# Kernel optimization log

Hardware: AMD Instinct MI355X
Metric: run time of the kernel (lower is better)

Reference implementation:

```python
import jax, jax.numpy as jnp
import numpy as np

B, T_DEC, T_ENC = 64, 400, 512
D = 256    # embed_size (GRU units, attention units, attention_layer_size)
PRE = 128  # prenet output dim (Tacotron prenet: 256 -> 128)
OUT = 400  # n_mels * r = 80 * 5


def _p(k, shape, s=0.05):
    return jax.random.normal(k, shape, dtype=jnp.float32) * s


def setup_inputs() -> dict:
    ks = jax.random.split(jax.random.key(0), 16)
    return {
        "dec_inputs": jax.random.normal(ks[0], (B, T_DEC, OUT), dtype=jnp.float32),
        "memory": jax.random.normal(ks[1], (B, T_ENC, D), dtype=jnp.float32),
        "W1": _p(ks[2], (OUT, D)), "b1": jnp.zeros((D,), jnp.float32),
        "W2": _p(ks[3], (D, PRE)), "b2": jnp.zeros((PRE,), jnp.float32),
        "k0": _p(ks[4], (PRE + D, 3 * D)), "r0": _p(ks[5], (D, 3 * D)),
        "bi0": jnp.zeros((3 * D,), jnp.float32), "br0": jnp.zeros((3 * D,), jnp.float32),
        "k1": _p(ks[6], (D, 3 * D)), "r1": _p(ks[7], (D, 3 * D)),
        "bi1": jnp.zeros((3 * D,), jnp.float32), "br1": jnp.zeros((3 * D,), jnp.float32),
        "Wq": _p(ks[8], (D, D)), "Wm": _p(ks[9], (D, D)), "v": _p(ks[10], (D,)),
        "Wa": _p(ks[11], (2 * D, D)),
        "Wo": _p(ks[12], (D, OUT)), "bo": jnp.zeros((OUT,), jnp.float32),
    }


def _gru(x, h, Wk, Wr, bi, br):
    # Keras GRUCell (reset_after=True)
    gx = x @ Wk + bi
    gh = h @ Wr + br
    xz, xr, xh = jnp.split(gx, 3, axis=-1)
    hz, hr, hh = jnp.split(gh, 3, axis=-1)
    z = jax.nn.sigmoid(xz + hz)
    r = jax.nn.sigmoid(xr + hr)
    hcand = jnp.tanh(xh + r * hh)
    return z * h + (1.0 - z) * hcand


def reference(dec_inputs, memory, W1, b1, W2, b2, k0, r0, bi0, br0,
              k1, r1, bi1, br1, Wq, Wm, v, Wa, Wo, bo):
    # Prenet (teacher forcing -> can apply to all steps up front). Dropout is
    # identity in eval mode.
    p = jax.nn.relu(jax.nn.relu(dec_inputs @ W1 + b1) @ W2 + b2)  # [B,Td,PRE]
    keys = memory @ Wm  # Bahdanau memory layer, precomputed  [B,Te,D]
    b = dec_inputs.shape[0]
    h0 = jnp.zeros((b, D), dec_inputs.dtype)
    h1 = jnp.zeros((b, D), dec_inputs.dtype)
    att0 = jnp.zeros((b, D), dec_inputs.dtype)

    def step(carry, x):
        h0, h1, att = carry
        cin = jnp.concatenate([x, att], axis=-1)           # [B, PRE+D]
        h0n = _gru(cin, h0, k0, r0, bi0, br0)
        h1n = _gru(h0n, h1, k1, r1, bi1, br1)              # cell output
        q = h1n @ Wq                                        # query layer
        score = jnp.einsum('btd,d->bt', jnp.tanh(keys + q[:, None, :]), v)
        alpha = jax.nn.softmax(score, axis=-1)              # [B,Te]
        ctx = jnp.einsum('bt,btd->bd', alpha, memory)       # context
        attn = jnp.concatenate([h1n, ctx], axis=-1) @ Wa    # attention layer
        y = attn @ Wo + bo                                  # output Dense
        return (h0n, h1n, attn), y

    _, ys = jax.lax.scan(step, (h0, h1, att0), jnp.swapaxes(p, 0, 1))
    return jnp.swapaxes(ys, 0, 1)  # [B, T_DEC, OUT]
```

## Files before the change

kernel.cpp:

```cpp
#include <hip/hip_runtime.h>
#include <hip/hip_fp16.h>

#define BB   64
#define TDEC 400
#define TENC 512
#define DD   256
#define PRE  128
#define NOUT 400
#define G3   768
#define C2E  2.8853900817779268f

typedef _Float16 h2_t __attribute__((ext_vector_type(2)));

__device__ __forceinline__ float fsig(float x) {
    return __builtin_amdgcn_rcpf(1.0f + __expf(-x));
}
__device__ __forceinline__ float ftanh(float x) {
    float t = __expf(2.0f * x);
    return 1.0f - 2.0f * __builtin_amdgcn_rcpf(t + 1.0f);
}
__device__ __forceinline__ float fexp2(float x) {
#if __has_builtin(__builtin_amdgcn_exp2f)
    return __builtin_amdgcn_exp2f(x);
#else
    return exp2f(x);
#endif
}
__device__ __forceinline__ float dot8(float4 w, float4 x, float acc) {
    union { float4 f; h2_t h[4]; } uw, ux;
    uw.f = w; ux.f = x;
#if __has_builtin(__builtin_amdgcn_fdot2)
    #pragma unroll
    for (int k = 0; k < 4; k++)
        acc = __builtin_amdgcn_fdot2(uw.h[k], ux.h[k], acc, false);
#else
    #pragma unroll
    for (int k = 0; k < 4; k++) {
        acc = fmaf((float)uw.h[k].x, (float)ux.h[k].x, acc);
        acc = fmaf((float)uw.h[k].y, (float)ux.h[k].y, acc);
    }
#endif
    return acc;
}

__global__ __launch_bounds__(256) void prenet_kernel(
    const float* __restrict__ x, const float* __restrict__ W1, const float* __restrict__ b1,
    const float* __restrict__ W2, const float* __restrict__ b2, __half* __restrict__ p_h)
{
    __shared__ __align__(16) float xs[8][NOUT];
    __shared__ __align__(16) float hs[8][DD];
    const int row0 = blockIdx.x * 8;
    const int tid = threadIdx.x;
    for (int idx = tid; idx < 8 * NOUT; idx += 256) {
        int m = idx / NOUT, i = idx - m * NOUT;
        xs[m][i] = x[(size_t)(row0 + m) * NOUT + i];
    }
    __syncthreads();
    {
        const int j = tid;
        float acc[8];
        float bj = b1[j];
        #pragma unroll
        for (int m = 0; m < 8; m++) acc[m] = bj;
        #pragma unroll 4
        for (int i = 0; i < NOUT; i++) {
            float w = W1[i * DD + j];
            #pragma unroll
            for (int m = 0; m < 8; m++) acc[m] = fmaf(xs[m][i], w, acc[m]);
        }
        #pragma unroll
        for (int m = 0; m < 8; m++) hs[m][j] = fmaxf(acc[m], 0.0f);
    }
    __syncthreads();
    if (tid < PRE) {
        const int j = tid;
        float acc[8];
        float bj = b2[j];
        #pragma unroll
        for (int m = 0; m < 8; m++) acc[m] = bj;
        #pragma unroll 4
        for (int i = 0; i < DD; i++) {
            float w = W2[i * PRE + j];
            #pragma unroll
            for (int m = 0; m < 8; m++) acc[m] = fmaf(hs[m][i], w, acc[m]);
        }
        #pragma unroll
        for (int m = 0; m < 8; m++)
            p_h[(size_t)(row0 + m) * PRE + j] = __float2half(fmaxf(acc[m], 0.0f));
    }
}

__global__ __launch_bounds__(768) void gx0_kernel(
    const __half* __restrict__ p_h, const float* __restrict__ k0,
    const float* __restrict__ bi0, __half* __restrict__ gxp)
{
    __shared__ __align__(16) float ps[8][PRE];
    const int row0 = blockIdx.x * 8;
    const int tid = threadIdx.x;
    for (int idx = tid; idx < 8 * PRE; idx += 768) {
        int m = idx >> 7, i = idx & 127;
        ps[m][i] = __half2float(p_h[(size_t)(row0 + m) * PRE + i]);
    }
    __syncthreads();
    const int j = tid;
    float acc[8];
    float bj = bi0[j];
    #pragma unroll
    for (int m = 0; m < 8; m++) acc[m] = bj;
    #pragma unroll 4
    for (int i = 0; i < PRE; i++) {
        float w = k0[(size_t)i * G3 + j];
        #pragma unroll
        for (int m = 0; m < 8; m++) acc[m] = fmaf(ps[m][i], w, acc[m]);
    }
    #pragma unroll
    for (int m = 0; m < 8; m++)
        gxp[(size_t)(row0 + m) * G3 + j] = __float2half(acc[m]);
}

__global__ __launch_bounds__(256) void keys_kernel(
    const float* __restrict__ mem, const float* __restrict__ Wm, __half* __restrict__ keys_p)
{
    __shared__ __align__(16) float xs[8][DD];
    const int row0 = blockIdx.x * 8;
    const int tid = threadIdx.x;
    for (int idx = tid; idx < 8 * DD; idx += 256) {
        int m = idx >> 8, i = idx & 255;
        xs[m][i] = mem[(size_t)(row0 + m) * DD + i];
    }
    __syncthreads();
    const int j = tid;
    const int i8 = j >> 3, k = j & 7;
    float acc[8] = {0.f,0.f,0.f,0.f,0.f,0.f,0.f,0.f};
    #pragma unroll 4
    for (int i = 0; i < DD; i++) {
        float w = Wm[i * DD + j];
        #pragma unroll
        for (int m = 0; m < 8; m++) acc[m] = fmaf(xs[m][i], w, acc[m]);
    }
    #pragma unroll
    for (int m = 0; m < 8; m++) {
        int r = row0 + m;
        int bb = r >> 9, e = r & 511;
        keys_p[(size_t)bb * (TENC * DD) + ((size_t)i8 * TENC + e) * 8 + k] =
            __float2half(C2E * acc[m]);
    }
}

__global__ __launch_bounds__(256) void pack_w_kernel(
    const float* __restrict__ src, __half* __restrict__ dst, int R, int C)
{
    int flat = blockIdx.x * 256 + threadIdx.x;
    if (flat < R * C) {
        int k = flat & 7;
        int t2 = flat >> 3;
        int j = t2 % C;
        int i8 = t2 / C;
        dst[flat] = __float2half(src[(size_t)(8 * i8 + k) * C + j]);
    }
}

__global__ __launch_bounds__(256) void pack_mem8_kernel(
    const float* __restrict__ mem, float4* __restrict__ dst)
{
    int flat = blockIdx.x * 256 + threadIdx.x;
    if (flat < BB * 64 * 256) {
        int d  = flat & 255;
        int e8 = (flat >> 8) & 63;
        int b  = flat >> 14;
        const float* base = mem + ((size_t)b * TENC + 8 * e8) * DD + d;
        union { float4 f; __half2 h[4]; } u;
        u.h[0] = __floats2half2_rn(base[0 * DD], base[1 * DD]);
        u.h[1] = __floats2half2_rn(base[2 * DD], base[3 * DD]);
        u.h[2] = __floats2half2_rn(base[4 * DD], base[5 * DD]);
        u.h[3] = __floats2half2_rn(base[6 * DD], base[7 * DD]);
        dst[flat] = u.f;
    }
}

__global__ __launch_bounds__(448) void out_kernel(
    const __half* __restrict__ ah, const float* __restrict__ Wo, const float* __restrict__ bo,
    float* __restrict__ y)
{
    __shared__ __align__(16) float xs[8][DD];
    const int row0 = blockIdx.x * 8;
    const int tid = threadIdx.x;
    for (int idx = tid; idx < 8 * DD; idx += 448) {
        int m = idx >> 8, i = idx & 255;
        xs[m][i] = __half2float(ah[(size_t)(row0 + m) * DD + i]);
    }
    __syncthreads();
    if (tid < NOUT) {
        const int j = tid;
        float acc[8];
        float bj = bo[j];
        #pragma unroll
        for (int m = 0; m < 8; m++) acc[m] = bj;
        #pragma unroll 4
        for (int i = 0; i < DD; i++) {
            float w = Wo[i * NOUT + j];
            #pragma unroll
            for (int m = 0; m < 8; m++) acc[m] = fmaf(xs[m][i], w, acc[m]);
        }
        #pragma unroll
        for (int m = 0; m < 8; m++) y[(size_t)(row0 + m) * NOUT + j] = acc[m];
    }
}

#define SCORE_BODY(UK) do {                                              \
    float4 q0 = qp4[2 * i8], q1 = qp4[2 * i8 + 1];                       \
    float4 v0 = vp4[2 * i8], v1 = vp4[2 * i8 + 1];                       \
    float a0 = (float)UK.h[0].x + q0.x;                                  \
    float a1 = (float)UK.h[0].y + q0.y;                                  \
    float a2 = (float)UK.h[1].x + q0.z;                                  \
    float a3 = (float)UK.h[1].y + q0.w;                                  \
    float a4 = (float)UK.h[2].x + q1.x;                                  \
    float a5 = (float)UK.h[2].y + q1.y;                                  \
    float a6 = (float)UK.h[3].x + q1.z;                                  \
    float a7 = (float)UK.h[3].y + q1.w;                                  \
    accA = fmaf(v0.x, __builtin_amdgcn_rcpf(fexp2(a0) + 1.0f), accA);    \
    accB = fmaf(v0.y, __builtin_amdgcn_rcpf(fexp2(a1) + 1.0f), accB);    \
    accA = fmaf(v0.z, __builtin_amdgcn_rcpf(fexp2(a2) + 1.0f), accA);    \
    accB = fmaf(v0.w, __builtin_amdgcn_rcpf(fexp2(a3) + 1.0f), accB);    \
    accA = fmaf(v1.x, __builtin_amdgcn_rcpf(fexp2(a4) + 1.0f), accA);    \
    accB = fmaf(v1.y, __builtin_amdgcn_rcpf(fexp2(a5) + 1.0f), accB);    \
    accA = fmaf(v1.z, __builtin_amdgcn_rcpf(fexp2(a6) + 1.0f), accA);    \
    accB = fmaf(v1.w, __builtin_amdgcn_rcpf(fexp2(a7) + 1.0f), accB);    \
} while (0)

__global__ __launch_bounds__(768, 1) void decoder_kernel(
    const __half* __restrict__ gxp,  const __half* __restrict__ keys_p,
    const float4* __restrict__ memq,
    const __half* __restrict__ k0p,  const __half* __restrict__ r0p,
    const __half* __restrict__ k1p,  const __half* __restrict__ r1p,
    const __half* __restrict__ Wqp,  const __half* __restrict__ Wap,
    const float* __restrict__ br0,
    const float* __restrict__ bi1, const float* __restrict__ br1,
    const float* __restrict__ v,   __half* __restrict__ ahist)
{
    __shared__ __align__(16) float4 kLds4[16 * TENC];
    __shared__ __align__(16) __half xa[DD];
    __shared__ __align__(16) __half h0s[DD], h1s[DD];
    __shared__ __align__(16) __half ctxh[DD];
    __shared__ __align__(16) float h0f[DD], h1f[DD];
    __shared__ __align__(16) float qf[DD], vf[DD];
    __shared__ __align__(16) float gx[G3], gh[G3];
    __shared__ __align__(16) float sc[TENC];
    __shared__ __align__(16) float hWa[DD];
    __shared__ __align__(16) float ctxp[3][DD];
    __shared__ __align__(16) float redd[16];

    const int tid = threadIdx.x;
    const int b = blockIdx.x;

    const float b0r_r = br0[tid];
    const float b1i_r = bi1[tid];
    const float b1r_r = br1[tid];
    if (tid < DD) {
        h0f[tid] = 0.0f; h1f[tid] = 0.0f;
        h0s[tid] = __float2half(0.0f); h1s[tid] = __float2half(0.0f);
        vf[tid] = v[tid];
        xa[tid] = __float2half(0.0f);
    }
    const __half*  keyb = keys_p + (size_t)b * TENC * DD;
    const float4*  kg4  = (const float4*)keyb;
    const float4*  mqb  = memq + (size_t)b * (TENC / 8) * DD;
    const __half*  gxb  = gxp + (size_t)b * TDEC * G3;

    {
        const float4* src = (const float4*)keyb;
        for (int idx = tid; idx < 16 * TENC; idx += 768)
            kLds4[idx] = src[16 * TENC + idx];
    }

    __half gpre = gxb[tid];
    __syncthreads();

    #pragma unroll 1
    for (int t = 0; t < TDEC; t++) {
        {
            const float4* wpA = (const float4*)k0p;
            const float4* wpB = (const float4*)r0p;
            const float4* xp  = (const float4*)xa;
            const float4* hp  = (const float4*)h0s;
            float acc  = __half2float(gpre);
            if (t + 1 < TDEC) gpre = gxb[(size_t)(t + 1) * G3 + tid];
            float acc2 = b0r_r;
            #pragma unroll 4
            for (int i8 = 0; i8 < 32; i8++) {
                float4 x = xp[i8], h = hp[i8];
                acc  = dot8(wpA[(16 + i8) * G3 + tid], x, acc);
                acc2 = dot8(wpB[i8 * G3 + tid], h, acc2);
            }
            gx[tid] = acc; gh[tid] = acc2;
        }
        __syncthreads();
        if (tid < DD) {
            float z = fsig(gx[tid] + gh[tid]);
            float r = fsig(gx[DD + tid] + gh[DD + tid]);
            float cand = ftanh(gx[2 * DD + tid] + r * gh[2 * DD + tid]);
            float hn = z * h0f[tid] + (1.0f - z) * cand;
            h0f[tid] = hn; h0s[tid] = __float2half(hn);
        }
        __syncthreads();

        {
            const float4* wpA = (const float4*)k1p;
            const float4* wpB = (const float4*)r1p;
            const float4* xp  = (const float4*)h0s;
            const float4* hp  = (const float4*)h1s;
            float acc  = b1i_r;
            float acc2 = b1r_r;
            #pragma unroll 4
            for (int i8 = 0; i8 < 32; i8++) {
                float4 x = xp[i8], h = hp[i8];
                acc  = dot8(wpA[i8 * G3 + tid], x, acc);
                acc2 = dot8(wpB[i8 * G3 + tid], h, acc2);
            }
            gx[tid] = acc; gh[tid] = acc2;
        }
        __syncthreads();
        if (tid < DD) {
            float z = fsig(gx[tid] + gh[tid]);
            float r = fsig(gx[DD + tid] + gh[DD + tid]);
            float cand = ftanh(gx[2 * DD + tid] + r * gh[2 * DD + tid]);
            float hn = z * h1f[tid] + (1.0f - z) * cand;
            h1f[tid] = hn; h1s[tid] = __float2half(hn);
        }
        __syncthreads();

        if (tid < 256) {
            const float4* wp = (const float4*)Wqp;
            const float4* hp = (const float4*)h1s;
            float a0 = 0.0f, a1 = 0.0f;
            #pragma unroll 4
            for (int i8 = 0; i8 < 32; i8 += 2) {
                a0 = dot8(wp[i8 * DD + tid], hp[i8], a0);
                a1 = dot8(wp[(i8 + 1) * DD + tid], hp[i8 + 1], a1);
            }
            qf[tid] = C2E * (a0 + a1);
        } else if (tid < 512) {
            const int d = tid - 256;
            const float4* wp = (const float4*)Wap;
            const float4* hp = (const float4*)h1s;
            float a0 = 0.0f, a1 = 0.0f;
            #pragma unroll 4
            for (int i8 = 0; i8 < 32; i8 += 2) {
                a0 = dot8(wp[i8 * DD + d], hp[i8], a0);
                a1 = dot8(wp[(i8 + 1) * DD + d], hp[i8 + 1], a1);
            }
            hWa[d] = a0 + a1;
        }
        __syncthreads();

        if (tid < TENC) {
            const float4* qp4 = (const float4*)qf;
            const float4* vp4 = (const float4*)vf;
            float accA = 0.0f, accB = 0.0f;
            #pragma unroll 8
            for (int i8 = 0; i8 < 16; i8++) {
                union { float4 f; h2_t h[4]; } uk;
                uk.f = kg4[i8 * TENC + tid];
                SCORE_BODY(uk);
            }
            #pragma unroll 4
            for (int i8 = 16; i8 < 32; i8++) {
                union { float4 f; h2_t h[4]; } uk;
                uk.f = kLds4[(i8 - 16) * TENC + tid];
                SCORE_BODY(uk);
            }
            float wv = __expf(-2.0f * (accA + accB));
            sc[tid] = wv;
            #pragma unroll
            for (int off = 32; off; off >>= 1) wv += __shfl_down(wv, off);
            if ((tid & 63) == 0) redd[tid >> 6] = wv;
        }
        __syncthreads();

        {
            const int d  = tid & 255;
            const int ch = tid >> 8;
            const int e8s = (ch == 0) ? 0 : (ch == 1) ? 22 : 43;
            const int e8e = (ch == 0) ? 22 : (ch == 1) ? 43 : 64;
            const float4* scp = (const float4*)sc;
            float acc = 0.0f;
            #pragma unroll 2
            for (int e8 = e8s; e8 < e8e; e8++) {
                union { float4 f; __half2 h[4]; } um;
                um.f = mqb[e8 * DD + d];
                float4 w0 = scp[2 * e8], w1 = scp[2 * e8 + 1];
                float2 f0 = __half22float2(um.h[0]), f1 = __half22float2(um.h[1]);
                float2 f2 = __half22float2(um.h[2]), f3 = __half22float2(um.h[3]);
                acc = fmaf(f0.x, w0.x, acc); acc = fmaf(f0.y, w0.y, acc);
                acc = fmaf(f1.x, w0.z, acc); acc = fmaf(f1.y, w0.w, acc);
                acc = fmaf(f2.x, w1.x, acc); acc = fmaf(f2.y, w1.y, acc);
                acc = fmaf(f3.x, w1.z, acc); acc = fmaf(f3.y, w1.w, acc);
            }
            ctxp[ch][d] = acc;
        }
        __syncthreads();

        if (tid < DD) {
            const float4* rp = (const float4*)redd;
            float4 ra = rp[0], rb = rp[1];
            float ssum = ((ra.x + ra.y) + (ra.z + ra.w)) + ((rb.x + rb.y) + (rb.z + rb.w));
            float c = (ctxp[0][tid] + ctxp[1][tid] + ctxp[2][tid]) * __builtin_amdgcn_rcpf(ssum);
            ctxh[tid] = __float2half(c);
        }
        __syncthreads();

        if (tid < DD) {
            const float4* wp = (const float4*)Wap;
            const float4* cp = (const float4*)ctxh;
            float a0 = hWa[tid], a1 = 0.0f;
            #pragma unroll 4
            for (int i8 = 0; i8 < 32; i8 += 2) {
                a0 = dot8(wp[(32 + i8) * DD + tid], cp[i8], a0);
                a1 = dot8(wp[(33 + i8) * DD + tid], cp[i8 + 1], a1);
            }
            __half ah = __float2half(a0 + a1);
            xa[tid] = ah;
            ahist[((size_t)b * TDEC + t) * DD + tid] = ah;
        }
        __syncthreads();
    }
}

extern "C" void kernel_launch(void* const* d_in, const int* in_sizes, int n_in,
                              void* d_out, int out_size, void* d_ws, size_t ws_size,
                              hipStream_t stream)
{
    const float* dec    = (const float*)d_in[0];
    const float* memory = (const float*)d_in[1];
    const float* W1  = (const float*)d_in[2];
    const float* b1  = (const float*)d_in[3];
    const float* W2  = (const float*)d_in[4];
    const float* b2  = (const float*)d_in[5];
    const float* k0  = (const float*)d_in[6];
    const float* r0  = (const float*)d_in[7];
    const float* bi0 = (const float*)d_in[8];
    const float* br0 = (const float*)d_in[9];
    const float* k1  = (const float*)d_in[10];
    const float* r1  = (const float*)d_in[11];
    const float* bi1 = (const float*)d_in[12];
    const float* br1 = (const float*)d_in[13];
    const float* Wq  = (const float*)d_in[14];
    const float* Wm  = (const float*)d_in[15];
    const float* v   = (const float*)d_in[16];
    const float* Wa  = (const float*)d_in[17];
    const float* Wo  = (const float*)d_in[18];
    const float* bo  = (const float*)d_in[19];
    float* out = (float*)d_out;
    (void)ws_size; (void)in_sizes; (void)n_in; (void)out_size;

    char* w = (char*)d_ws;
    size_t off = 0;
    __half*  p_h    = (__half*)(w + off);  off += (size_t)BB * TDEC * PRE * 2;
    __half*  keys_p = (__half*)(w + off);  off += (size_t)BB * TENC * DD * 2;
    float4*  memq   = (float4*)(w + off);  off += (size_t)BB * TENC * DD * 2;
    __half*  gxp    = (__half*)(w + off);  off += (size_t)BB * TDEC * G3 * 2;
    __half*  k0p    = (__half*)(w + off);  off += (size_t)384 * G3 * 2;
    __half*  r0p    = (__half*)(w + off);  off += (size_t)DD * G3 * 2;
    __half*  k1p    = (__half*)(w + off);  off += (size_t)DD * G3 * 2;
    __half*  r1p    = (__half*)(w + off);  off += (size_t)DD * G3 * 2;
    __half*  Wqp    = (__half*)(w + off);  off += (size_t)DD * DD * 2;
    __half*  Wap    = (__half*)(w + off);  off += (size_t)2 * DD * DD * 2;
    __half*  ahist  = (__half*)(w + off);  off += (size_t)BB * TDEC * DD * 2;

    prenet_kernel<<<BB * TDEC / 8, 256, 0, stream>>>(dec, W1, b1, W2, b2, p_h);
    gx0_kernel<<<BB * TDEC / 8, 768, 0, stream>>>(p_h, k0, bi0, gxp);
    keys_kernel<<<BB * TENC / 8, 256, 0, stream>>>(memory, Wm, keys_p);
    pack_mem8_kernel<<<(BB * 64 * 256) / 256, 256, 0, stream>>>(memory, memq);
    pack_w_kernel<<<(384 * G3 + 255) / 256, 256, 0, stream>>>(k0, k0p, 384, G3);
    pack_w_kernel<<<(DD * G3 + 255) / 256, 256, 0, stream>>>(r0, r0p, DD, G3);
    pack_w_kernel<<<(DD * G3 + 255) / 256, 256, 0, stream>>>(k1, k1p, DD, G3);
    pack_w_kernel<<<(DD * G3 + 255) / 256, 256, 0, stream>>>(r1, r1p, DD, G3);
    pack_w_kernel<<<(DD * DD + 255) / 256, 256, 0, stream>>>(Wq, Wqp, DD, DD);
    pack_w_kernel<<<(2 * DD * DD + 255) / 256, 256, 0, stream>>>(Wa, Wap, 2 * DD, DD);

    decoder_kernel<<<BB, 768, 0, stream>>>(gxp, keys_p, memq, k0p, r0p, k1p, r1p,
                                           Wqp, Wap, br0, bi1, br1, v, ahist);

    out_kernel<<<BB * TDEC / 8, 448, 0, stream>>>(ahist, Wo, bo, out);
}
```

Measured before the change: 14.28 ms.

## Split each batch decoder across two blocks exchanging partial context via global mailboxes

```diff
diff --git a/kernel.cpp b/kernel.cpp
--- a/kernel.cpp
+++ b/kernel.cpp
@@ -236,22 +236,29 @@
     const __half* __restrict__ Wqp,  const __half* __restrict__ Wap,
     const float* __restrict__ br0,
     const float* __restrict__ bi1, const float* __restrict__ br1,
-    const float* __restrict__ v,   __half* __restrict__ ahist)
-{
-    __shared__ __align__(16) float4 kLds4[16 * TENC];
+    const float* __restrict__ v,   __half* __restrict__ ahist,
+    float* __restrict__ mboxC, float* __restrict__ mboxS,
+    unsigned* __restrict__ flags)
+{
+    __shared__ __align__(16) float4 kAll[32 * 256];
     __shared__ __align__(16) __half xa[DD];
     __shared__ __align__(16) __half h0s[DD], h1s[DD];
     __shared__ __align__(16) __half ctxh[DD];
     __shared__ __align__(16) float h0f[DD], h1f[DD];
     __shared__ __align__(16) float qf[DD], vf[DD];
     __shared__ __align__(16) float gx[G3], gh[G3];
-    __shared__ __align__(16) float sc[TENC];
+    __shared__ __align__(16) float sc[256];
     __shared__ __align__(16) float hWa[DD];
     __shared__ __align__(16) float ctxp[3][DD];
-    __shared__ __align__(16) float redd[16];
+    __shared__ __align__(16) float redd[8];
 
     const int tid = threadIdx.x;
-    const int b = blockIdx.x;
+    const int idxb = blockIdx.x;
+    const int g    = idxb >> 4;
+    const int sub  = idxb & 15;
+    const int who  = sub >> 3;
+    const int b    = g * 8 + (sub & 7);
+    const int eBase = who * 256;
 
     const float b0r_r = br0[tid];
     const float b1i_r = bi1[tid];
@@ -267,10 +274,16 @@
     const float4*  mqb  = memq + (size_t)b * (TENC / 8) * DD;
     const __half*  gxb  = gxp + (size_t)b * TDEC * G3;
 
-    {
-        const float4* src = (const float4*)keyb;
-        for (int idx = tid; idx < 16 * TENC; idx += 768)
-            kLds4[idx] = src[16 * TENC + idx];
+    float* mcOwn  = mboxC + ((size_t)(b * 2 + who) * 2) * 256;
+    float* mcPeer = mboxC + ((size_t)(b * 2 + (who ^ 1)) * 2) * 256;
+    float* msOwn  = mboxS + (b * 2 + who) * 2;
+    float* msPeer = mboxS + (b * 2 + (who ^ 1)) * 2;
+    unsigned* flagOwn  = flags + (b * 2 + who);
+    unsigned* flagPeer = flags + (b * 2 + (who ^ 1));
+
+    for (int i2 = tid; i2 < 32 * 256; i2 += 768) {
+        int i8 = i2 >> 8, el = i2 & 255;
+        kAll[i2] = kg4[i8 * TENC + eBase + el];
     }
 
     __half gpre = gxb[tid];
@@ -353,24 +366,26 @@
         }
         __syncthreads();
 
-        if (tid < TENC) {
+        if (tid < 512) {
+            const int el   = tid >> 1;
+            const int half = tid & 1;
             const float4* qp4 = (const float4*)qf;
             const float4* vp4 = (const float4*)vf;
             float accA = 0.0f, accB = 0.0f;
+            const int i8s = half * 16;
             #pragma unroll 8
-            for (int i8 = 0; i8 < 16; i8++) {
+            for (int i8 = i8s; i8 < i8s + 16; i8++) {
                 union { float4 f; h2_t h[4]; } uk;
-                uk.f = kg4[i8 * TENC + tid];
+                uk.f = kAll[i8 * 256 + el];
                 SCORE_BODY(uk);
             }
-            #pragma unroll 4
-            for (int i8 = 16; i8 < 32; i8++) {
-                union { float4 f; h2_t h[4]; } uk;
-                uk.f = kLds4[(i8 - 16) * TENC + tid];
-                SCORE_BODY(uk);
-            }
-            float wv = __expf(-2.0f * (accA + accB));
-            sc[tid] = wv;
+            float tot = accA + accB;
+            tot += __shfl_xor(tot, 1);
+            float wv = 0.0f;
+            if (half == 0) {
+                wv = __expf(-2.0f * tot);
+                sc[el] = wv;
+            }
             #pragma unroll
             for (int off = 32; off; off >>= 1) wv += __shfl_down(wv, off);
             if ((tid & 63) == 0) redd[tid >> 6] = wv;
@@ -380,14 +395,14 @@
         {
             const int d  = tid & 255;
             const int ch = tid >> 8;
-            const int e8s = (ch == 0) ? 0 : (ch == 1) ? 22 : 43;
-            const int e8e = (ch == 0) ? 22 : (ch == 1) ? 43 : 64;
+            const int e8s = (ch == 0) ? 0 : (ch == 1) ? 11 : 22;
+            const int e8e = (ch == 0) ? 11 : (ch == 1) ? 22 : 32;
             const float4* scp = (const float4*)sc;
             float acc = 0.0f;
             #pragma unroll 2
             for (int e8 = e8s; e8 < e8e; e8++) {
                 union { float4 f; __half2 h[4]; } um;
-                um.f = mqb[e8 * DD + d];
+                um.f = mqb[(who * 32 + e8) * DD + d];
                 float4 w0 = scp[2 * e8], w1 = scp[2 * e8 + 1];
                 float2 f0 = __half22float2(um.h[0]), f1 = __half22float2(um.h[1]);
                 float2 f2 = __half22float2(um.h[2]), f3 = __half22float2(um.h[3]);
@@ -400,12 +415,31 @@
         }
         __syncthreads();
 
-        if (tid < DD) {
-            const float4* rp = (const float4*)redd;
-            float4 ra = rp[0], rb = rp[1];
-            float ssum = ((ra.x + ra.y) + (ra.z + ra.w)) + ((rb.x + rb.y) + (rb.z + rb.w));
-            float c = (ctxp[0][tid] + ctxp[1][tid] + ctxp[2][tid]) * __builtin_amdgcn_rcpf(ssum);
-            ctxh[tid] = __float2half(c);
+        const int par = t & 1;
+        float cOwn = 0.0f;
+        if (tid < 256) {
+            cOwn = ctxp[0][tid] + ctxp[1][tid] + ctxp[2][tid];
+            mcOwn[par * 256 + tid] = cOwn;
+        } else if (tid == 256) {
+            msOwn[par] = ((redd[0] + redd[1]) + (redd[2] + redd[3]))
+                       + ((redd[4] + redd[5]) + (redd[6] + redd[7]));
+        }
+        __syncthreads();
+        __threadfence();
+        if (tid == 0) {
+            atomicExch(flagOwn, (unsigned)(t + 1));
+            while (atomicAdd(flagPeer, 0u) < (unsigned)(t + 1))
+                __builtin_amdgcn_s_sleep(2);
+        }
+        __syncthreads();
+        __threadfence();
+        if (tid < 256) {
+            float cPeer = mcPeer[par * 256 + tid];
+            float sPeer = msPeer[par];
+            float sOwn  = ((redd[0] + redd[1]) + (redd[2] + redd[3]))
+                        + ((redd[4] + redd[5]) + (redd[6] + redd[7]));
+            float S = sOwn + sPeer;
+            ctxh[tid] = __float2half((cOwn + cPeer) * __builtin_amdgcn_rcpf(S));
         }
         __syncthreads();
 
@@ -420,7 +454,7 @@
             }
             __half ah = __float2half(a0 + a1);
             xa[tid] = ah;
-            ahist[((size_t)b * TDEC + t) * DD + tid] = ah;
+            if (who == 0) ahist[((size_t)b * TDEC + t) * DD + tid] = ah;
         }
         __syncthreads();
     }
@@ -467,6 +501,10 @@
     __half*  Wap    = (__half*)(w + off);  off += (size_t)2 * DD * DD * 2;
     __half*  ahist  = (__half*)(w + off);  off += (size_t)BB * TDEC * DD * 2;
 
+    float*    mboxC = (float*)p_h;
+    float*    mboxS = mboxC + (size_t)BB * 2 * 2 * 256;
+    unsigned* flags = (unsigned*)(mboxS + BB * 2 * 2);
+
     prenet_kernel<<<BB * TDEC / 8, 256, 0, stream>>>(dec, W1, b1, W2, b2, p_h);
     gx0_kernel<<<BB * TDEC / 8, 768, 0, stream>>>(p_h, k0, bi0, gxp);
     keys_kernel<<<BB * TENC / 8, 256, 0, stream>>>(memory, Wm, keys_p);
@@ -478,8 +516,11 @@
     pack_w_kernel<<<(DD * DD + 255) / 256, 256, 0, stream>>>(Wq, Wqp, DD, DD);
     pack_w_kernel<<<(2 * DD * DD + 255) / 256, 256, 0, stream>>>(Wa, Wap, 2 * DD, DD);
 
-    decoder_kernel<<<BB, 768, 0, stream>>>(gxp, keys_p, memq, k0p, r0p, k1p, r1p,
-                                           Wqp, Wap, br0, bi1, br1, v, ahist);
+    hipMemsetAsync(flags, 0, 2 * BB * sizeof(unsigned), stream);
+
+    decoder_kernel<<<2 * BB, 768, 0, stream>>>(gxp, keys_p, memq, k0p, r0p, k1p, r1p,
+                                               Wqp, Wap, br0, bi1, br1, v, ahist,
+                                               mboxC, mboxS, flags);
 
     out_kernel<<<BB * TDEC / 8, 448, 0, stream>>>(ahist, Wo, bo, out);
 }
```

Measured after the change: 27.45 ms. +92.3%, slower.
